# Optimization experiments

Hardware: AMD Instinct MI355X
Metric: run time of the kernel (lower is better)

Reference implementation:

```python
import jax, jax.numpy as jnp
import numpy as np

D_K = 512  # module-level global used for the scale factor


def setup_inputs() -> dict:
    key = jax.random.key(0)
    kq, kk, kv, km = jax.random.split(key, 4)
    B, H, L = 4, 8, 1024
    Q = jax.random.normal(kq, (B, H, L, D_K), dtype=jnp.float32)
    K = jax.random.normal(kk, (B, H, L, D_K), dtype=jnp.float32)
    V = jax.random.normal(kv, (B, H, L, D_K), dtype=jnp.float32)
    attn_mask = jax.random.randint(km, (B, H, L, L), 0, 2).astype(jnp.bool_)
    return {"Q": Q, "K": K, "V": V, "attn_mask": attn_mask}


def reference(Q, K, V, attn_mask):
    scale = 1.0 / np.sqrt(D_K).astype(np.float32)
    # [B,H,Lq,Lk]
    scores = jnp.einsum('bhqd,bhkd->bhqk', Q, K) * scale
    scores = jnp.where(attn_mask, jnp.float32(-1e9), scores)
    attn = jax.nn.softmax(scores, axis=-1)
    context = jnp.einsum('bhqk,bhkd->bhqd', attn, V)
    return (context, attn)
```

## Files before the change

kernel.cpp:

```cpp
#include <hip/hip_runtime.h>
#include <hip/hip_bf16.h>

constexpr int BH  = 32;
constexpr int LQ  = 1024;
constexpr int DK  = 512;
constexpr float SCALE = 0.04419417382415922f;

using short8 = __attribute__((ext_vector_type(8))) short;
using f32x4  = __attribute__((ext_vector_type(4))) float;

__device__ __forceinline__ unsigned short cvt_bf16(float x) {
  unsigned int u = __builtin_bit_cast(unsigned int, x);
  u += 0x7FFFu + ((u >> 16) & 1u);
  return (unsigned short)(u >> 16);
}
__device__ __forceinline__ float bf2f(unsigned short s) {
  return __builtin_bit_cast(float, (unsigned int)s << 16);
}
__device__ __forceinline__ unsigned int pack2(float a, float b) {
  return (unsigned int)cvt_bf16(a) | ((unsigned int)cvt_bf16(b) << 16);
}

__device__ __forceinline__ void lds_load16(const void* g, void* l) {
  __builtin_amdgcn_global_load_lds(
      (const __attribute__((address_space(1))) unsigned int*)g,
      (__attribute__((address_space(3))) unsigned int*)l, 16, 0, 0);
}

__global__ __launch_bounds__(256) void cvt2_f32_bf16(
    const float* __restrict__ s0, const float* __restrict__ s1,
    unsigned short* __restrict__ d0, unsigned short* __restrict__ d1, int n8) {
  const float* src = blockIdx.y ? s1 : s0;
  unsigned short* dst = blockIdx.y ? d1 : d0;
  int i = blockIdx.x * 256 + threadIdx.x;
  const int stride = gridDim.x * 256;
  for (; i < n8; i += stride) {
    float4 a = ((const float4*)src)[(size_t)i * 2];
    float4 b = ((const float4*)src)[(size_t)i * 2 + 1];
    unsigned short us[8] __attribute__((aligned(16)));
    us[0]=cvt_bf16(a.x); us[1]=cvt_bf16(a.y); us[2]=cvt_bf16(a.z); us[3]=cvt_bf16(a.w);
    us[4]=cvt_bf16(b.x); us[5]=cvt_bf16(b.y); us[6]=cvt_bf16(b.z); us[7]=cvt_bf16(b.w);
    ((short8*)dst)[i] = *(short8*)us;
  }
}

__global__ __launch_bounds__(512) void qk_v4_kernel(
    const unsigned short* __restrict__ A, const unsigned short* __restrict__ B,
    const int* __restrict__ mask, unsigned short* __restrict__ P,
    float* __restrict__ partials) {
  __shared__ __attribute__((aligned(16))) unsigned short smem[24576];

  int flat = blockIdx.x + 8 * (blockIdx.y + 4 * blockIdx.z);
  flat = (flat % 8) * 128 + flat / 8;
  const int bx = flat % 8;
  const int by = (flat / 8) % 4;
  const int bh = flat / 32;

  const int t = threadIdx.x;
  const int lane = t & 63, wave = t >> 6;
  const int wr = wave >> 1;
  const int wc = wave & 1;
  const int fr = lane & 15, fq = lane >> 4;
  const int m0 = by * 256, n0 = bx * 128;

  const char* Ab = (const char*)A + ((size_t)bh * LQ + m0) * 1024;
  const char* Bb = (const char*)B + ((size_t)bh * LQ + n0) * 1024;

  unsigned int orv = 0;
  {
    const unsigned int* mw = (const unsigned int*)mask;
    #pragma unroll
    for (int i = 0; i < 64; ++i) orv |= mw[i];
  }
  const bool byteMode = (orv > 1u);

  f32x4 acc[4][4];
  #pragma unroll
  for (int i = 0; i < 4; ++i)
    #pragma unroll
    for (int j = 0; j < 4; ++j) acc[i][j] = (f32x4){0.f, 0.f, 0.f, 0.f};

  char* const AsB = (char*)smem;
  char* const BsB = (char*)smem + 32768;

  for (int kt = 0; kt < 8; ++kt) {
    const int kb = kt * 128;
    __syncthreads();
    #pragma unroll
    for (int i = 0; i < 4; ++i) {
      const int p  = i * 8192 + t * 16;
      const int r  = p >> 7;
      const int ch = (p >> 4) & 7;
      lds_load16(Ab + (size_t)r * 1024 + kb + ((ch ^ (r & 7)) << 4),
                 AsB + i * 8192 + wave * 1024);
    }
    #pragma unroll
    for (int i = 0; i < 2; ++i) {
      const int p  = i * 8192 + t * 16;
      const int r  = p >> 7;
      const int ch = (p >> 4) & 7;
      lds_load16(Bb + (size_t)r * 1024 + kb + ((ch ^ (r & 7)) << 4),
                 BsB + i * 8192 + wave * 1024);
    }
    __syncthreads();

    #pragma unroll
    for (int kk = 0; kk < 2; ++kk) {
      short8 a[4], b[4];
      #pragma unroll
      for (int mi = 0; mi < 4; ++mi) {
        const int r  = wr * 64 + mi * 16 + fr;
        const int ch = (kk * 4 + fq) ^ (r & 7);
        a[mi] = *(const short8*)(AsB + r * 128 + ch * 16);
      }
      #pragma unroll
      for (int ni = 0; ni < 4; ++ni) {
        const int r  = wc * 64 + ni * 16 + fr;
        const int ch = (kk * 4 + fq) ^ (r & 7);
        b[ni] = *(const short8*)(BsB + r * 128 + ch * 16);
      }
      #pragma unroll
      for (int mi = 0; mi < 4; ++mi)
        #pragma unroll
        for (int ni = 0; ni < 4; ++ni)
          acc[mi][ni] = __builtin_amdgcn_mfma_f32_16x16x32_bf16(a[mi], b[ni], acc[mi][ni], 0, 0, 0);
    }
  }

  unsigned short* Cs = smem;
  const size_t pbase = (size_t)bh * LQ * LQ;
  #pragma unroll
  for (int h = 0; h < 2; ++h) {
    __syncthreads();
    if ((wr >> 1) == h) {
      #pragma unroll
      for (int mi = 0; mi < 4; ++mi)
        #pragma unroll
        for (int ni = 0; ni < 4; ++ni) {
          const int col = wc * 64 + ni * 16 + fr;
          #pragma unroll
          for (int r = 0; r < 4; ++r) {
            const int rloc = (wr & 1) * 64 + mi * 16 + fq * 4 + r;
            Cs[rloc * 136 + col] = cvt_bf16(__expf(acc[mi][ni][r] * SCALE));
          }
        }
    }
    __syncthreads();
    const int rl = t >> 4;
    const int cl = (t & 15) * 8;
    #pragma unroll
    for (int rb = 0; rb < 4; ++rb) {
      const int rloc = rb * 32 + rl;
      const int rg   = m0 + h * 128 + rloc;
      const size_t gidx = pbase + (size_t)rg * LQ + (n0 + cl);
      short8 sv = *(const short8*)&Cs[rloc * 136 + cl];
      bool mk[8];
      if (byteMode) {
        const unsigned char* mb = (const unsigned char*)mask + gidx;
        uint2 w = *(const uint2*)mb;
        #pragma unroll
        for (int j = 0; j < 4; ++j) mk[j]     = ((w.x >> (8 * j)) & 255u) != 0u;
        #pragma unroll
        for (int j = 0; j < 4; ++j) mk[4 + j] = ((w.y >> (8 * j)) & 255u) != 0u;
      } else {
        int4 w0 = *(const int4*)(mask + gidx);
        int4 w1 = *(const int4*)(mask + gidx + 4);
        mk[0] = w0.x != 0; mk[1] = w0.y != 0; mk[2] = w0.z != 0; mk[3] = w0.w != 0;
        mk[4] = w1.x != 0; mk[5] = w1.y != 0; mk[6] = w1.z != 0; mk[7] = w1.w != 0;
      }
      unsigned short out[8] __attribute__((aligned(16)));
      float s = 0.f;
      #pragma unroll
      for (int j = 0; j < 8; ++j) {
        unsigned short v = mk[j] ? (unsigned short)0 : (unsigned short)sv[j];
        out[j] = v;
        s += bf2f(v);
      }
      *(short8*)(P + gidx) = *(short8*)out;
      s += __shfl_xor(s, 1); s += __shfl_xor(s, 2);
      s += __shfl_xor(s, 4); s += __shfl_xor(s, 8);
      if ((t & 15) == 0)
        partials[((size_t)bh * LQ + rg) * 8 + bx] = s;
    }
  }
}

__global__ __launch_bounds__(256) void attn_fin(
    const unsigned short* __restrict__ P, const float* __restrict__ partials,
    float* __restrict__ attn) {
  const int ch = blockIdx.x, rb64 = blockIdx.y, bh = blockIdx.z;
  const int m0 = rb64 * 64;
  __shared__ float invs[64];
  const int t = threadIdx.x;
  if (t < 64) {
    const float* pp = partials + ((size_t)bh * LQ + m0 + t) * 8;
    float s = ((pp[0] + pp[1]) + (pp[2] + pp[3])) + ((pp[4] + pp[5]) + (pp[6] + pp[7]));
    invs[t] = 1.0f / s;
  }
  __syncthreads();
  const size_t pbase = (size_t)bh * LQ * LQ;
  const int c0 = ch * 512;
  #pragma unroll
  for (int rb = 0; rb < 4; ++rb) {
    const int rloc = rb * 16 + (t >> 4);
    const int row  = m0 + rloc;
    const float inv = invs[rloc];
    const size_t base = pbase + (size_t)row * LQ + c0 + (t & 15) * 8;
    #pragma unroll
    for (int j = 0; j < 4; ++j) {
      short8 sv = *(const short8*)(P + base + j * 128);
      float4 o0, o1;
      o0.x = bf2f((unsigned short)sv[0]) * inv;
      o0.y = bf2f((unsigned short)sv[1]) * inv;
      o0.z = bf2f((unsigned short)sv[2]) * inv;
      o0.w = bf2f((unsigned short)sv[3]) * inv;
      o1.x = bf2f((unsigned short)sv[4]) * inv;
      o1.y = bf2f((unsigned short)sv[5]) * inv;
      o1.z = bf2f((unsigned short)sv[6]) * inv;
      o1.w = bf2f((unsigned short)sv[7]) * inv;
      *(float4*)(attn + base + j * 128)     = o0;
      *(float4*)(attn + base + j * 128 + 4) = o1;
    }
  }
}

__global__ __launch_bounds__(256) void pv2_kernel(
    const unsigned short* __restrict__ P, const float* __restrict__ V,
    const float* __restrict__ partials, float* __restrict__ O) {
  __shared__ __attribute__((aligned(16))) unsigned short As[8192];
  __shared__ __attribute__((aligned(16))) unsigned short BsV[128 * 72];
  __shared__ float invsL[128];

  int flat = blockIdx.x + 4 * (blockIdx.y + 8 * blockIdx.z);
  flat = (flat % 8) * 128 + flat / 8;
  const int bx = flat % 4;
  const int by = (flat / 4) % 8;
  const int bh = flat / 32;

  const int t = threadIdx.x;
  const int lane = t & 63, wave = t >> 6;
  const int wr = wave >> 1, wc = wave & 1;
  const int fr = lane & 15, fq = lane >> 4;
  const int m0 = by * 128, n0 = bx * 128;

  if (t < 128) {
    const float* pp = partials + ((size_t)bh * LQ + m0 + t) * 8;
    float s = ((pp[0] + pp[1]) + (pp[2] + pp[3])) + ((pp[4] + pp[5]) + (pp[6] + pp[7]));
    invsL[t] = 1.0f / s;
  }

  const char* Ab  = (const char*)P + ((size_t)bh * LQ + m0) * 2048;
  const float* Vb = V + (size_t)bh * LQ * DK + n0;

  f32x4 acc[4][4];
  #pragma unroll
  for (int i = 0; i < 4; ++i)
    #pragma unroll
    for (int j = 0; j < 4; ++j) acc[i][j] = (f32x4){0.f, 0.f, 0.f, 0.f};

  const int g  = t >> 5;
  const int nl = t & 31;

  for (int k0 = 0; k0 < LQ; k0 += 64) {
    __syncthreads();
    #pragma unroll
    for (int i = 0; i < 4; ++i) {
      const int p  = i * 4096 + t * 16;
      const int r  = p >> 7;
      const int ch = (p >> 4) & 7;
      const int sw = ((ch ^ (r & 7)) << 4);
      lds_load16(Ab + (size_t)r * 2048 + k0 * 2 + sw, (char*)As + wave * 1024 + i * 4096);
    }
    float vf[8][4];
    #pragma unroll
    for (int i = 0; i < 8; ++i) {
      const size_t rb = (size_t)(k0 + 8 * g + i) * DK;
      #pragma unroll
      for (int jn = 0; jn < 4; ++jn)
        vf[i][jn] = Vb[rb + nl + 32 * jn];
    }
    #pragma unroll
    for (int jn = 0; jn < 4; ++jn) {
      const int n = nl + 32 * jn;
      uint2 w0, w1;
      w0.x = pack2(vf[0][jn], vf[1][jn]); w0.y = pack2(vf[2][jn], vf[3][jn]);
      w1.x = pack2(vf[4][jn], vf[5][jn]); w1.y = pack2(vf[6][jn], vf[7][jn]);
      *(uint2*)((char*)BsV + n * 144 + 16 * g)     = w0;
      *(uint2*)((char*)BsV + n * 144 + 16 * g + 8) = w1;
    }
    __syncthreads();

    #pragma unroll
    for (int kk = 0; kk < 2; ++kk) {
      short8 a[4], b[4];
      #pragma unroll
      for (int mi = 0; mi < 4; ++mi) {
        const int r  = wr * 64 + mi * 16 + fr;
        const int ch = (kk * 4 + fq) ^ (r & 7);
        a[mi] = *(const short8*)((const char*)As + r * 128 + ch * 16);
      }
      #pragma unroll
      for (int ni = 0; ni < 4; ++ni) {
        const int r = wc * 64 + ni * 16 + fr;
        b[ni] = *(const short8*)((const char*)BsV + r * 144 + (kk * 4 + fq) * 16);
      }
      #pragma unroll
      for (int mi = 0; mi < 4; ++mi)
        #pragma unroll
        for (int ni = 0; ni < 4; ++ni)
          acc[mi][ni] = __builtin_amdgcn_mfma_f32_16x16x32_bf16(a[mi], b[ni], acc[mi][ni], 0, 0, 0);
    }
  }

  const size_t obase = (size_t)bh * LQ * DK;
  #pragma unroll
  for (int mi = 0; mi < 4; ++mi)
    #pragma unroll
    for (int ni = 0; ni < 4; ++ni) {
      const int col = n0 + wc * 64 + ni * 16 + fr;
      #pragma unroll
      for (int r = 0; r < 4; ++r) {
        const int rloc = wr * 64 + mi * 16 + fq * 4 + r;
        O[obase + (size_t)(m0 + rloc) * DK + col] = acc[mi][ni][r] * invsL[rloc];
      }
    }
}

__global__ __launch_bounds__(256) void qk_mask_kernel(
    const float* __restrict__ Q, const float* __restrict__ Kmat,
    const int* __restrict__ mask, float* __restrict__ S) {
  __shared__ __attribute__((aligned(16))) unsigned short Asf[128][40];
  __shared__ __attribute__((aligned(16))) unsigned short Bsf[128][40];
  const int t = threadIdx.x;
  const int lane = t & 63, wave = t >> 6;
  const int wr = wave >> 1, wc = wave & 1;
  const int fr = lane & 15, fq = lane >> 4;
  const int bh = blockIdx.z;
  const int m0 = blockIdx.y * 128, n0 = blockIdx.x * 128;
  const float* Qb = Q + (size_t)bh * LQ * DK;
  const float* Kb = Kmat + (size_t)bh * LQ * DK;
  unsigned int orv = 0;
  { const unsigned int* mw = (const unsigned int*)mask;
    #pragma unroll
    for (int i = 0; i < 64; ++i) orv |= mw[i]; }
  const bool byteMode = (orv > 1u);
  f32x4 acc[4][4];
  #pragma unroll
  for (int i = 0; i < 4; ++i)
    #pragma unroll
    for (int j = 0; j < 4; ++j) acc[i][j] = (f32x4){0.f,0.f,0.f,0.f};
  const int sr = t >> 1, sc = (t & 1) * 16;
  for (int kd = 0; kd < DK; kd += 32) {
    __syncthreads();
    { const float4* qa = (const float4*)(Qb + (size_t)(m0+sr)*DK + kd + sc);
      float fv[16];
      #pragma unroll
      for (int i = 0; i < 4; ++i) { float4 x = qa[i];
        fv[4*i]=x.x; fv[4*i+1]=x.y; fv[4*i+2]=x.z; fv[4*i+3]=x.w; }
      unsigned short us[16] __attribute__((aligned(16)));
      #pragma unroll
      for (int i = 0; i < 16; ++i) us[i] = cvt_bf16(fv[i]);
      *(short8*)&Asf[sr][sc]   = *(short8*)&us[0];
      *(short8*)&Asf[sr][sc+8] = *(short8*)&us[8]; }
    { const float4* ka = (const float4*)(Kb + (size_t)(n0+sr)*DK + kd + sc);
      float fv[16];
      #pragma unroll
      for (int i = 0; i < 4; ++i) { float4 x = ka[i];
        fv[4*i]=x.x; fv[4*i+1]=x.y; fv[4*i+2]=x.z; fv[4*i+3]=x.w; }
      unsigned short us[16] __attribute__((aligned(16)));
      #pragma unroll
      for (int i = 0; i < 16; ++i) us[i] = cvt_bf16(fv[i]);
      *(short8*)&Bsf[sr][sc]   = *(short8*)&us[0];
      *(short8*)&Bsf[sr][sc+8] = *(short8*)&us[8]; }
    __syncthreads();
    short8 a[4], b[4];
    #pragma unroll
    for (int mi = 0; mi < 4; ++mi) a[mi] = *(const short8*)&Asf[wr*64+mi*16+fr][fq*8];
    #pragma unroll
    for (int ni = 0; ni < 4; ++ni) b[ni] = *(const short8*)&Bsf[wc*64+ni*16+fr][fq*8];
    #pragma unroll
    for (int mi = 0; mi < 4; ++mi)
      #pragma unroll
      for (int ni = 0; ni < 4; ++ni)
        acc[mi][ni] = __builtin_amdgcn_mfma_f32_16x16x32_bf16(a[mi], b[ni], acc[mi][ni], 0, 0, 0);
  }
  const size_t sbase = (size_t)bh * LQ * LQ;
  const unsigned char* mb = (const unsigned char*)mask;
  #pragma unroll
  for (int mi = 0; mi < 4; ++mi)
    #pragma unroll
    for (int ni = 0; ni < 4; ++ni) {
      const int col = n0 + wc*64 + ni*16 + fr;
      #pragma unroll
      for (int r = 0; r < 4; ++r) {
        const int row = m0 + wr*64 + mi*16 + fq*4 + r;
        const size_t idx = sbase + (size_t)row * LQ + col;
        float s = acc[mi][ni][r] * SCALE;
        const bool msk = byteMode ? (mb[idx] != 0) : (mask[idx] != 0);
        S[idx] = msk ? -1e9f : s;
      }
    }
}

__global__ __launch_bounds__(256) void softmax_kernel(float* __restrict__ A) {
  const int row = blockIdx.x;
  float4* rp = (float4*)(A + (size_t)row * LQ);
  const int t = threadIdx.x;
  float4 v = rp[t];
  float m = fmaxf(fmaxf(v.x, v.y), fmaxf(v.z, v.w));
  #pragma unroll
  for (int off = 32; off >= 1; off >>= 1) m = fmaxf(m, __shfl_xor(m, off, 64));
  __shared__ float redm[4];
  const int wv = t >> 6, ln = t & 63;
  if (ln == 0) redm[wv] = m;
  __syncthreads();
  m = fmaxf(fmaxf(redm[0], redm[1]), fmaxf(redm[2], redm[3]));
  float4 e;
  e.x = expf(v.x - m); e.y = expf(v.y - m); e.z = expf(v.z - m); e.w = expf(v.w - m);
  float s = (e.x + e.y) + (e.z + e.w);
  #pragma unroll
  for (int off = 32; off >= 1; off >>= 1) s += __shfl_xor(s, off, 64);
  __shared__ float reds2[4];
  if (ln == 0) reds2[wv] = s;
  __syncthreads();
  s = (reds2[0] + reds2[1]) + (reds2[2] + reds2[3]);
  const float inv = 1.0f / s;
  e.x *= inv; e.y *= inv; e.z *= inv; e.w *= inv;
  rp[t] = e;
}

__global__ __launch_bounds__(256) void pv_kernel(
    const float* __restrict__ P, const float* __restrict__ V, float* __restrict__ O) {
  __shared__ __attribute__((aligned(16))) unsigned short Ps[128][40];
  __shared__ __attribute__((aligned(16))) unsigned short Vtl[128][40];
  const int t = threadIdx.x;
  const int lane = t & 63, wave = t >> 6;
  const int wr = wave >> 1, wc = wave & 1;
  const int fr = lane & 15, fq = lane >> 4;
  const int bh = blockIdx.z;
  const int m0 = blockIdx.y * 128, n0 = blockIdx.x * 128;
  const float* Pb = P + (size_t)bh * LQ * LQ;
  const float* Vb = V + (size_t)bh * LQ * DK;
  f32x4 acc[4][4];
  #pragma unroll
  for (int i = 0; i < 4; ++i)
    #pragma unroll
    for (int j = 0; j < 4; ++j) acc[i][j] = (f32x4){0.f,0.f,0.f,0.f};
  const int sr = t >> 1, sc = (t & 1) * 16;
  const int kk = (t & 15) * 2, nn = (t >> 4) * 8;
  for (int k0 = 0; k0 < LQ; k0 += 32) {
    __syncthreads();
    { const float4* pa = (const float4*)(Pb + (size_t)(m0+sr)*LQ + k0 + sc);
      float fv[16];
      #pragma unroll
      for (int i = 0; i < 4; ++i) { float4 x = pa[i];
        fv[4*i]=x.x; fv[4*i+1]=x.y; fv[4*i+2]=x.z; fv[4*i+3]=x.w; }
      unsigned short us[16] __attribute__((aligned(16)));
      #pragma unroll
      for (int i = 0; i < 16; ++i) us[i] = cvt_bf16(fv[i]);
      *(short8*)&Ps[sr][sc]   = *(short8*)&us[0];
      *(short8*)&Ps[sr][sc+8] = *(short8*)&us[8]; }
    { const float* v0p = Vb + (size_t)(k0+kk)*DK + n0 + nn;
      const float* v1p = v0p + DK;
      float4 a0 = *(const float4*)v0p, a1 = *(const float4*)(v0p+4);
      float4 b0 = *(const float4*)v1p, b1 = *(const float4*)(v1p+4);
      float r0[8] = {a0.x,a0.y,a0.z,a0.w,a1.x,a1.y,a1.z,a1.w};
      float r1[8] = {b0.x,b0.y,b0.z,b0.w,b1.x,b1.y,b1.z,b1.w};
      #pragma unroll
      for (int i = 0; i < 8; ++i) {
        unsigned int pk = (unsigned int)cvt_bf16(r0[i]) | ((unsigned int)cvt_bf16(r1[i]) << 16);
        *(unsigned int*)&Vtl[nn+i][kk] = pk; } }
    __syncthreads();
    short8 a[4], b[4];
    #pragma unroll
    for (int mi = 0; mi < 4; ++mi) a[mi] = *(const short8*)&Ps[wr*64+mi*16+fr][fq*8];
    #pragma unroll
    for (int ni = 0; ni < 4; ++ni) b[ni] = *(const short8*)&Vtl[wc*64+ni*16+fr][fq*8];
    #pragma unroll
    for (int mi = 0; mi < 4; ++mi)
      #pragma unroll
      for (int ni = 0; ni < 4; ++ni)
        acc[mi][ni] = __builtin_amdgcn_mfma_f32_16x16x32_bf16(a[mi], b[ni], acc[mi][ni], 0, 0, 0);
  }
  const size_t obase = (size_t)bh * LQ * DK;
  #pragma unroll
  for (int mi = 0; mi < 4; ++mi)
    #pragma unroll
    for (int ni = 0; ni < 4; ++ni) {
      const int col = n0 + wc*64 + ni*16 + fr;
      #pragma unroll
      for (int r = 0; r < 4; ++r) {
        const int row = m0 + wr*64 + mi*16 + fq*4 + r;
        O[obase + (size_t)row * DK + col] = acc[mi][ni][r];
      }
    }
}

extern "C" void kernel_launch(void* const* d_in, const int* in_sizes, int n_in,
                              void* d_out, int out_size, void* d_ws, size_t ws_size,
                              hipStream_t stream) {
  const float* Q    = (const float*)d_in[0];
  const float* K    = (const float*)d_in[1];
  const float* V    = (const float*)d_in[2];
  const int*   mask = (const int*)d_in[3];

  float* ctx  = (float*)d_out;
  float* attn = ctx + (size_t)BH * LQ * DK;

  const size_t NE = (size_t)BH * LQ * DK;
  const size_t P_BYTES  = (size_t)BH * LQ * LQ * 2;
  const size_t WS_NEED  = P_BYTES + (size_t)BH * LQ * 8 * 4;

  if (ws_size >= WS_NEED) {
    unsigned short* Pp       = (unsigned short*)d_ws;
    float*          partials = (float*)((char*)d_ws + P_BYTES);
    unsigned short* Qb = (unsigned short*)ctx;
    unsigned short* Kb = Qb + NE;

    cvt2_f32_bf16<<<dim3(1024, 2), 256, 0, stream>>>(Q, K, Qb, Kb, (int)(NE / 8));
    qk_v4_kernel<<<dim3(8, 4, BH), 512, 0, stream>>>(Qb, Kb, mask, Pp, partials);
    attn_fin<<<dim3(2, 16, BH), 256, 0, stream>>>(Pp, partials, attn);
    pv2_kernel<<<dim3(4, 8, BH), 256, 0, stream>>>(Pp, V, partials, ctx);
  } else {
    qk_mask_kernel<<<dim3(8, 8, BH), 256, 0, stream>>>(Q, K, mask, attn);
    softmax_kernel<<<dim3(BH * LQ), 256, 0, stream>>>(attn);
    pv_kernel<<<dim3(4, 8, BH), 256, 0, stream>>>(attn, V, ctx);
  }
}
```

Baseline: 225.6 us.

## Fuse fp32-to-bf16 conversion of Q/K into QK GEMM tile loads

Removes the separate Q/K conversion kernel and its bf16 round-trip through global memory. The QK kernel now reads fp32 Q and K directly, converts them to bf16 in registers with the hardware packed-convert instruction, and writes the result into the swizzled LDS tiles. The asynchronous global-to-LDS loads are replaced by register loads plus LDS stores. Each tile therefore pulls twice the bytes from global memory, and Q/K are re-read once per output tile instead of once in total. The V packing in the PV kernel also switches to the hardware convert.

```diff
diff --git a/kernel.cpp b/kernel.cpp
--- a/kernel.cpp
+++ b/kernel.cpp
@@ -17,8 +17,10 @@
 __device__ __forceinline__ float bf2f(unsigned short s) {
   return __builtin_bit_cast(float, (unsigned int)s << 16);
 }
-__device__ __forceinline__ unsigned int pack2(float a, float b) {
-  return (unsigned int)cvt_bf16(a) | ((unsigned int)cvt_bf16(b) << 16);
+__device__ __forceinline__ unsigned int pkbf(float lo, float hi) {
+  unsigned int r;
+  asm volatile("v_cvt_pk_bf16_f32 %0, %1, %2" : "=v"(r) : "v"(lo), "v"(hi));
+  return r;
 }
 
 __device__ __forceinline__ void lds_load16(const void* g, void* l) {
@@ -27,25 +29,8 @@
       (__attribute__((address_space(3))) unsigned int*)l, 16, 0, 0);
 }
 
-__global__ __launch_bounds__(256) void cvt2_f32_bf16(
-    const float* __restrict__ s0, const float* __restrict__ s1,
-    unsigned short* __restrict__ d0, unsigned short* __restrict__ d1, int n8) {
-  const float* src = blockIdx.y ? s1 : s0;
-  unsigned short* dst = blockIdx.y ? d1 : d0;
-  int i = blockIdx.x * 256 + threadIdx.x;
-  const int stride = gridDim.x * 256;
-  for (; i < n8; i += stride) {
-    float4 a = ((const float4*)src)[(size_t)i * 2];
-    float4 b = ((const float4*)src)[(size_t)i * 2 + 1];
-    unsigned short us[8] __attribute__((aligned(16)));
-    us[0]=cvt_bf16(a.x); us[1]=cvt_bf16(a.y); us[2]=cvt_bf16(a.z); us[3]=cvt_bf16(a.w);
-    us[4]=cvt_bf16(b.x); us[5]=cvt_bf16(b.y); us[6]=cvt_bf16(b.z); us[7]=cvt_bf16(b.w);
-    ((short8*)dst)[i] = *(short8*)us;
-  }
-}
-
-__global__ __launch_bounds__(512) void qk_v4_kernel(
-    const unsigned short* __restrict__ A, const unsigned short* __restrict__ B,
+__global__ __launch_bounds__(512) void qk_v5_kernel(
+    const float* __restrict__ Q, const float* __restrict__ K,
     const int* __restrict__ mask, unsigned short* __restrict__ P,
     float* __restrict__ partials) {
   __shared__ __attribute__((aligned(16))) unsigned short smem[24576];
@@ -63,8 +48,8 @@
   const int fr = lane & 15, fq = lane >> 4;
   const int m0 = by * 256, n0 = bx * 128;
 
-  const char* Ab = (const char*)A + ((size_t)bh * LQ + m0) * 1024;
-  const char* Bb = (const char*)B + ((size_t)bh * LQ + n0) * 1024;
+  const float* Ab = Q + ((size_t)bh * LQ + m0) * DK;
+  const float* Bb = K + ((size_t)bh * LQ + n0) * DK;
 
   unsigned int orv = 0;
   {
@@ -84,23 +69,33 @@
   char* const BsB = (char*)smem + 32768;
 
   for (int kt = 0; kt < 8; ++kt) {
-    const int kb = kt * 128;
+    const int kf = kt * 64;
     __syncthreads();
     #pragma unroll
     for (int i = 0; i < 4; ++i) {
       const int p  = i * 8192 + t * 16;
       const int r  = p >> 7;
       const int ch = (p >> 4) & 7;
-      lds_load16(Ab + (size_t)r * 1024 + kb + ((ch ^ (r & 7)) << 4),
-                 AsB + i * 8192 + wave * 1024);
+      const int sw = ch ^ (r & 7);
+      const float4* src = (const float4*)(Ab + (size_t)r * DK + kf + sw * 8);
+      float4 x = src[0], y = src[1];
+      uint4 w;
+      w.x = pkbf(x.x, x.y); w.y = pkbf(x.z, x.w);
+      w.z = pkbf(y.x, y.y); w.w = pkbf(y.z, y.w);
+      *(uint4*)(AsB + i * 8192 + t * 16) = w;
     }
     #pragma unroll
     for (int i = 0; i < 2; ++i) {
       const int p  = i * 8192 + t * 16;
       const int r  = p >> 7;
       const int ch = (p >> 4) & 7;
-      lds_load16(Bb + (size_t)r * 1024 + kb + ((ch ^ (r & 7)) << 4),
-                 BsB + i * 8192 + wave * 1024);
+      const int sw = ch ^ (r & 7);
+      const float4* src = (const float4*)(Bb + (size_t)r * DK + kf + sw * 8);
+      float4 x = src[0], y = src[1];
+      uint4 w;
+      w.x = pkbf(x.x, x.y); w.y = pkbf(x.z, x.w);
+      w.z = pkbf(y.x, y.y); w.w = pkbf(y.z, y.w);
+      *(uint4*)(BsB + i * 8192 + t * 16) = w;
     }
     __syncthreads();
 
@@ -283,8 +278,8 @@
     for (int jn = 0; jn < 4; ++jn) {
       const int n = nl + 32 * jn;
       uint2 w0, w1;
-      w0.x = pack2(vf[0][jn], vf[1][jn]); w0.y = pack2(vf[2][jn], vf[3][jn]);
-      w1.x = pack2(vf[4][jn], vf[5][jn]); w1.y = pack2(vf[6][jn], vf[7][jn]);
+      w0.x = pkbf(vf[0][jn], vf[1][jn]); w0.y = pkbf(vf[2][jn], vf[3][jn]);
+      w1.x = pkbf(vf[4][jn], vf[5][jn]); w1.y = pkbf(vf[6][jn], vf[7][jn]);
       *(uint2*)((char*)BsV + n * 144 + 16 * g)     = w0;
       *(uint2*)((char*)BsV + n * 144 + 16 * g + 8) = w1;
     }
@@ -507,18 +502,14 @@
   float* ctx  = (float*)d_out;
   float* attn = ctx + (size_t)BH * LQ * DK;
 
-  const size_t NE = (size_t)BH * LQ * DK;
   const size_t P_BYTES  = (size_t)BH * LQ * LQ * 2;
   const size_t WS_NEED  = P_BYTES + (size_t)BH * LQ * 8 * 4;
 
   if (ws_size >= WS_NEED) {
     unsigned short* Pp       = (unsigned short*)d_ws;
     float*          partials = (float*)((char*)d_ws + P_BYTES);
-    unsigned short* Qb = (unsigned short*)ctx;
-    unsigned short* Kb = Qb + NE;
-
-    cvt2_f32_bf16<<<dim3(1024, 2), 256, 0, stream>>>(Q, K, Qb, Kb, (int)(NE / 8));
-    qk_v4_kernel<<<dim3(8, 4, BH), 512, 0, stream>>>(Qb, Kb, mask, Pp, partials);
+
+    qk_v5_kernel<<<dim3(8, 4, BH), 512, 0, stream>>>(Q, K, mask, Pp, partials);
     attn_fin<<<dim3(2, 16, BH), 256, 0, stream>>>(Pp, partials, attn);
     pv2_kernel<<<dim3(4, 8, BH), 256, 0, stream>>>(Pp, V, partials, ctx);
   } else {
```

After: 242.8 us. 1.08x slower.
